# Optimization experiments

Hardware: AMD Instinct MI355X
Metric: run time of the kernel (lower is better)

The kernel has to match this reference:

```python
import jax, jax.numpy as jnp
import numpy as np

DIM = 768
NUM_HEADS = 12
HEAD_DIM = DIM // NUM_HEADS
SCALE = HEAD_DIM ** -0.5


def setup_inputs() -> dict:
    key = jax.random.key(0)
    k1, k2, k3, k4 = jax.random.split(key, 4)
    B, H, W = 8, 32, 32
    x = jax.random.normal(k1, (B, H, W, DIM), dtype=jnp.float32)
    s = DIM ** -0.5
    w_qkv = jax.random.normal(k2, (DIM, 3 * DIM), dtype=jnp.float32) * s
    w_proj = jax.random.normal(k3, (DIM, DIM), dtype=jnp.float32) * s
    b_proj = jax.random.normal(k4, (DIM,), dtype=jnp.float32) * 0.01
    return {"x": x, "w_qkv": w_qkv, "w_proj": w_proj, "b_proj": b_proj}


def reference(x, w_qkv, w_proj, b_proj):
    B, H, W, C = x.shape
    N = H * W
    qkv = (x.reshape(B, N, C) @ w_qkv).reshape(B, N, 3, NUM_HEADS, HEAD_DIM)
    q, k, v = jnp.moveaxis(qkv, 2, 0)  # each (B, N, h, d)
    # scores: (B, h, N, N)
    attn = jnp.einsum('bnhd,bmhd->bhnm', q * SCALE, k)
    attn = jax.nn.softmax(attn, axis=-1)
    out = jnp.einsum('bhnm,bmhd->bnhd', attn, v).reshape(B, H, W, C)
    return out @ w_proj + b_proj
```

## Files before the change

### kernel.cpp

```cpp
#include <hip/hip_runtime.h>

typedef _Float16 half_t;
typedef __attribute__((ext_vector_type(4))) _Float16 half4;
typedef __attribute__((ext_vector_type(8))) _Float16 half8;
typedef __attribute__((ext_vector_type(4))) float floatx4;

#define MFMA_F16(A,B,C)  __builtin_amdgcn_mfma_f32_16x16x32_f16(A,B,C,0,0,0)
#define MFMA16(A,B,C)    __builtin_amdgcn_mfma_f32_16x16x16f16(A,B,C,0,0,0)

typedef __attribute__((address_space(1))) const void gvoid_t;
typedef __attribute__((address_space(3))) void svoid_t;

__device__ __forceinline__ void async_copy16(const half_t* g, half_t* l) {
    __builtin_amdgcn_global_load_lds((gvoid_t*)g, (svoid_t*)l, 16, 0, 0);
}

__global__ __launch_bounds__(256)
void prep_kernel(const float* __restrict__ x, const float* __restrict__ w_qkv,
                 const float* __restrict__ w_proj, half_t* __restrict__ xh,
                 half_t* __restrict__ wqkvT, half_t* __restrict__ wprojT)
{
    __shared__ half_t tile[64 * 65];
    const int id = blockIdx.x, tid = threadIdx.x;
    if (id < 6144) {
        size_t e = (size_t)id * 1024 + tid * 4;
        float4 f = *(const float4*)(x + e);
        half4 h = { (half_t)f.x, (half_t)f.y, (half_t)f.z, (half_t)f.w };
        *(half4*)(xh + e) = h;
        return;
    }
    const float* src; half_t* dst; int lds, tr0, tc0;
    if (id < 6576) { int t = id - 6144; src = w_qkv; dst = wqkvT; lds = 2304;
                     tr0 = (t / 36) * 64; tc0 = (t % 36) * 64; }
    else           { int t = id - 6576; src = w_proj; dst = wprojT; lds = 768;
                     tr0 = (t / 12) * 64; tc0 = (t % 12) * 64; }
    #pragma unroll
    for (int i = 0; i < 4; i++) {
        int e = tid + i * 256, r = e >> 4, c4 = (e & 15) << 2;
        float4 f = *(const float4*)(src + (size_t)(tr0 + r) * lds + tc0 + c4);
        tile[(c4 + 0) * 65 + r] = (half_t)f.x;
        tile[(c4 + 1) * 65 + r] = (half_t)f.y;
        tile[(c4 + 2) * 65 + r] = (half_t)f.z;
        tile[(c4 + 3) * 65 + r] = (half_t)f.w;
    }
    __syncthreads();
    #pragma unroll
    for (int i = 0; i < 4; i++) {
        int e = tid + i * 256, c = e >> 4, r4 = (e & 15) << 2;
        half4 h = { tile[c * 65 + r4], tile[c * 65 + r4 + 1],
                    tile[c * 65 + r4 + 2], tile[c * 65 + r4 + 3] };
        *(half4*)(dst + (size_t)(tc0 + c) * 768 + tr0 + r4) = h;
    }
}

template<int MODE>
__global__ __launch_bounds__(256, 2)
void gemm_kernel(const half_t* __restrict__ A, const half_t* __restrict__ Bt,
                 half_t* __restrict__ q_ws, half_t* __restrict__ k_ws,
                 half_t* __restrict__ v_ws,
                 float* __restrict__ Cout, const float* __restrict__ bias,
                 int M, int N, int K)
{
    __shared__ half_t As[128 * 64];
    __shared__ half_t Bs[128 * 64];

    const int tid  = threadIdx.x;
    const int lane = tid & 63;
    const int w    = tid >> 6;
    const int wm   = w >> 1, wn = w & 1;
    const int quad = lane >> 4, l16 = lane & 15;
    const int m0 = blockIdx.y * 128, n0 = blockIdx.x * 128;

    const int lrow = lane >> 3;
    const int lcc  = (lane & 7) ^ lrow;
    const half_t* Ag = A  + (size_t)(m0 + w * 32 + lrow) * K + lcc * 8;
    const half_t* Bg = Bt + (size_t)(n0 + w * 32 + lrow) * K + lcc * 8;

    floatx4 acc[4][4];
    #pragma unroll
    for (int i = 0; i < 4; i++)
        #pragma unroll
        for (int j = 0; j < 4; j++) acc[i][j] = (floatx4)0.0f;

    const int xsw = l16 & 7;

    for (int k0 = 0; k0 < K; k0 += 64) {
        #pragma unroll
        for (int i = 0; i < 4; i++) {
            async_copy16(Ag + (size_t)(i * 8) * K + k0, As + (w * 4 + i) * 512);
            async_copy16(Bg + (size_t)(i * 8) * K + k0, Bs + (w * 4 + i) * 512);
        }
        __syncthreads();

        #pragma unroll
        for (int ks = 0; ks < 2; ks++) {
            half8 a[4], b[4];
            #pragma unroll
            for (int mi = 0; mi < 4; mi++)
                a[mi] = *(const half8*)(As + (wm * 64 + mi * 16 + l16) * 64
                                           + (((ks << 2) + quad) ^ xsw) * 8);
            #pragma unroll
            for (int ni = 0; ni < 4; ni++)
                b[ni] = *(const half8*)(Bs + (wn * 64 + ni * 16 + l16) * 64
                                           + (((ks << 2) + quad) ^ xsw) * 8);
            #pragma unroll
            for (int mi = 0; mi < 4; mi++)
                #pragma unroll
                for (int ni = 0; ni < 4; ni++)
                    acc[mi][ni] = MFMA_F16(a[mi], b[ni], acc[mi][ni]);
        }
        __syncthreads();
    }

    if constexpr (MODE == 0) {
        const int sel  = n0 / 768;
        const int rem0 = n0 - sel * 768;
        #pragma unroll
        for (int mi = 0; mi < 4; mi++) {
            #pragma unroll
            for (int ni = 0; ni < 4; ni++) {
                int gnr = rem0 + wn * 64 + ni * 16 + l16;
                int h = gnr >> 6, d = gnr & 63;
                #pragma unroll
                for (int r = 0; r < 4; r++) {
                    int gm = m0 + wm * 64 + mi * 16 + quad * 4 + r;
                    int bb = gm >> 10, tok = gm & 1023;
                    size_t base = (size_t)(bb * 12 + h) * 65536;
                    float val = acc[mi][ni][r];
                    if (sel == 0)      q_ws[base + (size_t)tok * 64 + d] = (half_t)(val * 0.125f);
                    else if (sel == 1) k_ws[base + (size_t)tok * 64 + d] = (half_t)val;
                    else               v_ws[base + (size_t)d * 1024 + tok] = (half_t)val;
                }
            }
        }
    } else {
        #pragma unroll
        for (int mi = 0; mi < 4; mi++)
            #pragma unroll
            for (int ni = 0; ni < 4; ni++) {
                int gn = n0 + wn * 64 + ni * 16 + l16;
                #pragma unroll
                for (int r = 0; r < 4; r++) {
                    int gm = m0 + wm * 64 + mi * 16 + quad * 4 + r;
                    Cout[(size_t)gm * N + gn] = acc[mi][ni][r] + bias[gn];
                }
            }
    }
}

__global__ __launch_bounds__(256, 3)
void attn_kernel(const half_t* __restrict__ q, const half_t* __restrict__ k,
                 const half_t* __restrict__ vT, half_t* __restrict__ a_ws)
{
    __shared__ __align__(16) half_t Kb[2][4096];
    __shared__ __align__(16) half_t Vb[2][4096];

    const int tid  = threadIdx.x;
    const int lane = tid & 63;
    const int w    = tid >> 6;
    const int quad = lane >> 4, l16 = lane & 15;
    const int qc = blockIdx.x;
    const int bh = blockIdx.y;

    const half_t* kg = k  + (size_t)bh * 65536;
    const half_t* vg = vT + (size_t)bh * 65536;

    const int srow = lane >> 3;
    const int sch  = (lane & 7) ^ srow;

    const half_t* qp = q + ((size_t)bh * 1024 + qc * 128 + w * 16 + l16) * 64;
    half8 qf[2][2];
    #pragma unroll
    for (int T = 0; T < 2; T++)
        #pragma unroll
        for (int ks = 0; ks < 2; ks++)
            qf[T][ks] = *(const half8*)(qp + T * 4096 + ks * 32 + quad * 8);

    floatx4 acc_o[2][4];
    floatx4 lacc[2];
    #pragma unroll
    for (int T = 0; T < 2; T++) {
        lacc[T] = (floatx4)0.0f;
        #pragma unroll
        for (int dt = 0; dt < 4; dt++) acc_o[T][dt] = (floatx4)0.0f;
    }

    const int xsw = l16 & 7;
    const half4 vone = { (half_t)1.0f, (half_t)1.0f, (half_t)1.0f, (half_t)1.0f };

    #pragma unroll
    for (int j = 0; j < 2; j++) {
        int row = j * 32 + w * 8;
        async_copy16(kg + (size_t)(row + srow) * 64 + sch * 8, &Kb[0][row * 64]);
        async_copy16(vg + (size_t)(row + srow) * 1024 + sch * 8, &Vb[0][row * 64]);
    }

    for (int kt = 0; kt < 16; kt++) {
        const int cb = kt & 1;
        __syncthreads();
        if (kt < 15) {
            #pragma unroll
            for (int j = 0; j < 2; j++) {
                int row = j * 32 + w * 8;
                async_copy16(kg + (size_t)((kt + 1) * 64 + row + srow) * 64 + sch * 8,
                             &Kb[cb ^ 1][row * 64]);
                async_copy16(vg + (size_t)(row + srow) * 1024 + (kt + 1) * 64 + sch * 8,
                             &Vb[cb ^ 1][row * 64]);
            }
        }
        const half_t* Kc = Kb[cb];
        const half_t* Vc = Vb[cb];

        floatx4 sc[2][4];
        #pragma unroll
        for (int T = 0; T < 2; T++)
            #pragma unroll
            for (int mt = 0; mt < 4; mt++) sc[T][mt] = (floatx4)0.0f;
        #pragma unroll
        for (int ks = 0; ks < 2; ks++)
            #pragma unroll
            for (int mt = 0; mt < 4; mt++) {
                half8 kf = *(const half8*)(Kc + (mt * 16 + l16) * 64
                                              + (((ks << 2) + quad) ^ xsw) * 8);
                sc[0][mt] = MFMA_F16(kf, qf[0][ks], sc[0][mt]);
                sc[1][mt] = MFMA_F16(kf, qf[1][ks], sc[1][mt]);
            }

        half4 pa[2][4];
        #pragma unroll
        for (int T = 0; T < 2; T++)
            #pragma unroll
            for (int mt = 0; mt < 4; mt++) {
                half4 ph;
                #pragma unroll
                for (int r = 0; r < 4; r++) ph[r] = (half_t)__expf(sc[T][mt][r]);
                pa[T][mt] = ph;
            }

        #pragma unroll
        for (int kst = 0; kst < 4; kst++) {
            lacc[0] = MFMA16(pa[0][kst], vone, lacc[0]);
            lacc[1] = MFMA16(pa[1][kst], vone, lacc[1]);
            #pragma unroll
            for (int dt = 0; dt < 4; dt++) {
                int row = dt * 16 + l16;
                half4 vb4 = *(const half4*)(Vc + row * 64
                              + ((((kst << 1) + (quad >> 1)) ^ xsw) << 3)
                              + ((quad & 1) << 2));
                acc_o[0][dt] = MFMA16(pa[0][kst], vb4, acc_o[0][dt]);
                acc_o[1][dt] = MFMA16(pa[1][kst], vb4, acc_o[1][dt]);
            }
        }
    }

    const int b = bh / 12, h = bh - (bh / 12) * 12;
    #pragma unroll
    for (int T = 0; T < 2; T++)
        #pragma unroll
        for (int r = 0; r < 4; r++) {
            float inv = 1.0f / lacc[T][r];
            int n = qc * 128 + T * 64 + w * 16 + quad * 4 + r;
            half_t* op = a_ws + ((size_t)(b * 1024 + n)) * 768 + h * 64;
            #pragma unroll
            for (int dt = 0; dt < 4; dt++)
                op[dt * 16 + l16] = (half_t)(acc_o[T][dt][r] * inv);
        }
}

extern "C" void kernel_launch(void* const* d_in, const int* in_sizes, int n_in,
                              void* d_out, int out_size, void* d_ws, size_t ws_size,
                              hipStream_t stream)
{
    (void)in_sizes; (void)n_in; (void)out_size; (void)ws_size;
    const float* x      = (const float*)d_in[0];
    const float* w_qkv  = (const float*)d_in[1];
    const float* w_proj = (const float*)d_in[2];
    const float* b_proj = (const float*)d_in[3];
    float* out = (float*)d_out;

    half_t* ws     = (half_t*)d_ws;
    half_t* q_ws   = ws;
    half_t* k_ws   = ws + 6291456;
    half_t* v_ws   = ws + 2 * 6291456;
    half_t* xh     = ws + 3 * 6291456;
    half_t* wqkvT  = ws + 4 * 6291456;
    half_t* wprojT = wqkvT + 1769472;
    half_t* a_ws   = xh;

    prep_kernel<<<dim3(6720), dim3(256), 0, stream>>>(x, w_qkv, w_proj, xh, wqkvT, wprojT);
    gemm_kernel<0><<<dim3(18, 64), dim3(256), 0, stream>>>(
        xh, wqkvT, q_ws, k_ws, v_ws, nullptr, nullptr, 8192, 2304, 768);
    attn_kernel<<<dim3(8, 96), dim3(256), 0, stream>>>(q_ws, k_ws, v_ws, a_ws);
    gemm_kernel<1><<<dim3(6, 64), dim3(256), 0, stream>>>(
        a_ws, wprojT, nullptr, nullptr, nullptr, out, b_proj, 8192, 768, 768);
}
```

Measured before the change: 212.9 us.

## Use 16x16x32 MFMA for PV by permuting V token layout

Replaces the 16x16x16 MFMAs in the P·V and row-sum step with 16x16x32 MFMAs. Two score tiles are packed into one 8-wide fp16 operand, which halves the MFMA count and the number of V LDS reads. To make the K-dimension ordering match, the QKV GEMM epilogue now writes V tokens in a permuted order inside each 32-token group. This relies on the permutation matching the score accumulator layout exactly, and it makes the scattered V stores slightly more complex.

```diff
diff --git a/kernel.cpp b/kernel.cpp
--- a/kernel.cpp
+++ b/kernel.cpp
@@ -6,7 +6,6 @@
 typedef __attribute__((ext_vector_type(4))) float floatx4;
 
 #define MFMA_F16(A,B,C)  __builtin_amdgcn_mfma_f32_16x16x32_f16(A,B,C,0,0,0)
-#define MFMA16(A,B,C)    __builtin_amdgcn_mfma_f32_16x16x16f16(A,B,C,0,0,0)
 
 typedef __attribute__((address_space(1))) const void gvoid_t;
 typedef __attribute__((address_space(3))) void svoid_t;
@@ -129,7 +128,10 @@
                     float val = acc[mi][ni][r];
                     if (sel == 0)      q_ws[base + (size_t)tok * 64 + d] = (half_t)(val * 0.125f);
                     else if (sel == 1) k_ws[base + (size_t)tok * 64 + d] = (half_t)val;
-                    else               v_ws[base + (size_t)d * 1024 + tok] = (half_t)val;
+                    else {
+                        int tokp = (tok & ~31) | (quad << 3) | ((mi & 1) << 2) | r;
+                        v_ws[base + (size_t)d * 1024 + tokp] = (half_t)val;
+                    }
                 }
             }
         }
@@ -186,7 +188,8 @@
     }
 
     const int xsw = l16 & 7;
-    const half4 vone = { (half_t)1.0f, (half_t)1.0f, (half_t)1.0f, (half_t)1.0f };
+    const half8 vone = { (half_t)1.0f, (half_t)1.0f, (half_t)1.0f, (half_t)1.0f,
+                         (half_t)1.0f, (half_t)1.0f, (half_t)1.0f, (half_t)1.0f };
 
     #pragma unroll
     for (int j = 0; j < 2; j++) {
@@ -226,29 +229,29 @@
                 sc[1][mt] = MFMA_F16(kf, qf[1][ks], sc[1][mt]);
             }
 
-        half4 pa[2][4];
+        half8 pa[2][2];
         #pragma unroll
         for (int T = 0; T < 2; T++)
             #pragma unroll
-            for (int mt = 0; mt < 4; mt++) {
-                half4 ph;
-                #pragma unroll
-                for (int r = 0; r < 4; r++) ph[r] = (half_t)__expf(sc[T][mt][r]);
-                pa[T][mt] = ph;
-            }
-
-        #pragma unroll
-        for (int kst = 0; kst < 4; kst++) {
-            lacc[0] = MFMA16(pa[0][kst], vone, lacc[0]);
-            lacc[1] = MFMA16(pa[1][kst], vone, lacc[1]);
+            for (int g = 0; g < 2; g++) {
+                half8 ph;
+                #pragma unroll
+                for (int r = 0; r < 4; r++) ph[r]     = (half_t)__expf(sc[T][2 * g][r]);
+                #pragma unroll
+                for (int r = 0; r < 4; r++) ph[4 + r] = (half_t)__expf(sc[T][2 * g + 1][r]);
+                pa[T][g] = ph;
+            }
+
+        #pragma unroll
+        for (int g = 0; g < 2; g++) {
+            lacc[0] = MFMA_F16(pa[0][g], vone, lacc[0]);
+            lacc[1] = MFMA_F16(pa[1][g], vone, lacc[1]);
             #pragma unroll
             for (int dt = 0; dt < 4; dt++) {
-                int row = dt * 16 + l16;
-                half4 vb4 = *(const half4*)(Vc + row * 64
-                              + ((((kst << 1) + (quad >> 1)) ^ xsw) << 3)
-                              + ((quad & 1) << 2));
-                acc_o[0][dt] = MFMA16(pa[0][kst], vb4, acc_o[0][dt]);
-                acc_o[1][dt] = MFMA16(pa[1][kst], vb4, acc_o[1][dt]);
+                half8 vb = *(const half8*)(Vc + (dt * 16 + l16) * 64
+                                              + ((((g << 2) + quad) ^ xsw) << 3));
+                acc_o[0][dt] = MFMA_F16(pa[0][g], vb, acc_o[0][dt]);
+                acc_o[1][dt] = MFMA_F16(pa[1][g], vb, acc_o[1][dt]);
             }
         }
     }
```

After: 210.4 us. Within noise of the previous version (-1.2%).
